# Optimization experiments

Measured on AMD Instinct MI355X. Metric: run time of the kernel, lower is better.

The kernel has to match this reference:

```python
import jax, jax.numpy as jnp
import numpy as np
from jax.scipy.special import logsumexp

NUM_CLASSES = 2
THRESHOLD = 0.35      # overlap_thresh
NEGPOS_RATIO = 7      # neg_pos
VAR0, VAR1 = 0.1, 0.2  # self.variance


def point_form(p):
    # (cx,cy,w,h) -> (x1,y1,x2,y2)
    return jnp.concatenate([p[:, :2] - p[:, 2:] / 2, p[:, :2] + p[:, 2:] / 2], axis=1)


def jaccard(a, b):
    # a: [T,4] xyxy, b: [P,4] xyxy -> IoU [T,P]
    lt = jnp.maximum(a[:, None, :2], b[None, :, :2])
    rb = jnp.minimum(a[:, None, 2:], b[None, :, 2:])
    wh = jnp.clip(rb - lt, 0.0)
    inter = wh[..., 0] * wh[..., 1]
    area_a = ((a[:, 2] - a[:, 0]) * (a[:, 3] - a[:, 1]))[:, None]
    area_b = ((b[:, 2] - b[:, 0]) * (b[:, 3] - b[:, 1]))[None, :]
    return inter / (area_a + area_b - inter)


def encode(matched, priors):
    # matched xyxy [P,4], priors cxcywh [P,4]
    g_cxcy = ((matched[:, :2] + matched[:, 2:]) / 2 - priors[:, :2]) / (VAR0 * priors[:, 2:])
    g_wh = jnp.log((matched[:, 2:] - matched[:, :2]) / priors[:, 2:]) / VAR1
    return jnp.concatenate([g_cxcy, g_wh], axis=1)


def encode_landm(matched, priors):
    m = matched.reshape(-1, 5, 2)  # [P,5,2]
    g = (m - priors[:, None, :2]) / (VAR0 * priors[:, None, 2:])
    return g.reshape(-1, 10)


def match_one(truths, labels, landms, priors):
    # truths [T,4] xyxy, labels [T], landms [T,10], priors [P,4] cxcywh
    overlaps = jaccard(truths, point_form(priors))  # [T,P]
    best_prior_overlap = overlaps.max(axis=1)       # [T]
    best_prior_idx = overlaps.argmax(axis=1)        # [T]
    valid_gt = best_prior_overlap >= 0.2            # hard-gt filter
    best_truth_overlap = overlaps.max(axis=0)       # [P]
    best_truth_idx = overlaps.argmax(axis=0)        # [P]
    # index_fill_(0, best_prior_idx[valid], 2): IoU <= 1 so scatter-max is exact
    best_truth_overlap = best_truth_overlap.at[best_prior_idx].max(
        jnp.where(valid_gt, 2.0, 0.0))
    best_truth_idx = best_truth_idx.at[best_prior_idx].set(jnp.arange(truths.shape[0]))
    matches = truths[best_truth_idx]                # [P,4]
    conf = jnp.where(best_truth_overlap < THRESHOLD, 0.0, labels[best_truth_idx])
    loc = encode(matches, priors)
    landm = encode_landm(landms[best_truth_idx], priors)
    any_valid = valid_gt.any()                      # early-return branch in torch match()
    loc = jnp.where(any_valid, loc, 0.0)
    conf = jnp.where(any_valid, conf, 0.0)
    landm = jnp.where(any_valid, landm, 0.0)
    return loc, conf.astype(jnp.int32), landm


def smooth_l1(x):
    ax = jnp.abs(x)
    return jnp.where(ax < 1.0, 0.5 * ax * ax, ax - 0.5)


def multibox_loss(loc_data, conf_data, landm_data, priors, targets):
    num_priors = priors.shape[0]
    # torch uses .data (detached) for matching/encoding targets
    truths = jax.lax.stop_gradient(targets[..., :4])
    landms_gt = jax.lax.stop_gradient(targets[..., 4:14])
    labels = jax.lax.stop_gradient(targets[..., 14])
    pri = jax.lax.stop_gradient(priors)
    loc_t, conf_t, landm_t = jax.vmap(match_one, in_axes=(0, 0, 0, None))(
        truths, labels, landms_gt, pri)  # [B,P,4], [B,P], [B,P,10]

    # landmark loss over conf_t > 0
    pos1 = conf_t > 0
    N1 = jnp.maximum(pos1.sum().astype(jnp.float32), 1.0)
    loss_landm = jnp.sum(smooth_l1(landm_data - landm_t) * pos1[..., None])

    # localization loss over conf_t != 0; conf_t[pos] = 1
    pos = conf_t != 0
    conf_t = jnp.where(pos, 1, conf_t)
    loss_l = jnp.sum(smooth_l1(loc_data - loc_t) * pos[..., None])

    # per-prior CE = logsumexp(logits) - logit[target]
    ce = logsumexp(conf_data, axis=-1) - jnp.take_along_axis(
        conf_data, conf_t[..., None], axis=-1)[..., 0]  # [B,P]
    # hard negative mining: zero positives, double-argsort rank trick
    rank_loss = jnp.where(pos, 0.0, ce)
    idx_rank = jnp.argsort(jnp.argsort(-rank_loss, axis=1), axis=1)
    num_pos = pos.sum(axis=1, keepdims=True)
    num_neg = jnp.minimum(NEGPOS_RATIO * num_pos, num_priors - 1)
    neg = idx_rank < num_neg
    loss_c = jnp.sum(jnp.where(pos | neg, ce, 0.0))

    N = jnp.maximum(num_pos.sum().astype(jnp.float32), 1.0)
    return loss_l / N, loss_c / N, loss_landm / N1


def setup_inputs() -> dict:
    key = jax.random.key(0)
    ks = jax.random.split(key, 8)
    B, P, T = 16, 32768, 64
    loc_data = jax.random.normal(ks[0], (B, P, 4), jnp.float32)
    conf_data = jax.random.normal(ks[1], (B, P, NUM_CLASSES), jnp.float32)
    landm_data = jax.random.normal(ks[2], (B, P, 10), jnp.float32)
    # priors: (cx,cy,w,h), all positive and in (0,1)
    cxcy = jax.random.uniform(ks[3], (P, 2), minval=0.05, maxval=0.95)
    wh = jax.random.uniform(ks[4], (P, 2), minval=0.02, maxval=0.3)
    priors = jnp.concatenate([cxcy, wh], axis=1)
    # targets: [x1,y1,x2,y2, 10 landmark coords, label]
    c = jax.random.uniform(ks[5], (B, T, 2), minval=0.15, maxval=0.85)
    s = jax.random.uniform(ks[6], (B, T, 2), minval=0.05, maxval=0.25)
    boxes = jnp.concatenate([c - s / 2, c + s / 2], axis=-1)
    lm = jax.random.uniform(ks[7], (B, T, 10))
    labels = jnp.ones((B, T, 1), jnp.float32)
    targets = jnp.concatenate([boxes, lm, labels], axis=-1)
    return {"loc_data": loc_data, "conf_data": conf_data,
            "landm_data": landm_data, "priors": priors, "targets": targets}


def reference(loc_data, conf_data, landm_data, priors, targets):
    return multibox_loss(loc_data, conf_data, landm_data, priors, targets)
```

## Files before the change

kernel.cpp:

```cpp
#include <hip/hip_runtime.h>
#include <math.h>

#define OVERLAP_THRESH 0.35f
#define VALID_THRESH   0.2f
#define NEGPOS         7
#define TMAX           64
#define NCHUNK         16
#define TPW            4
#define EPT            4
#define HB             2048
#define NC             4
#define NSCAN          32

__device__ __forceinline__ float sl1(float x) {
    float ax = fabsf(x);
    return ax < 1.0f ? 0.5f * ax * ax : ax - 0.5f;
}
__device__ __forceinline__ float frcp(float x) { return __builtin_amdgcn_rcpf(x); }

__device__ __forceinline__ void atomicMaxU8(unsigned char* addr, unsigned char val) {
    size_t a = (size_t)addr;
    unsigned* word = (unsigned*)(a & ~(size_t)3);
    int shift = (int)(a & 3) * 8;
    unsigned old = *word, assumed;
    do {
        unsigned cur = (old >> shift) & 0xFFu;
        if (cur >= val) break;
        assumed = old;
        unsigned nw = (old & ~(0xFFu << shift)) | ((unsigned)val << shift);
        old = atomicCAS(word, assumed, nw);
    } while (old != assumed);
}

__global__ void clear_ws_kernel(uint4* __restrict__ p, size_t n16) {
    size_t i = (size_t)blockIdx.x * blockDim.x + threadIdx.x;
    size_t stride = (size_t)gridDim.x * blockDim.x;
    uint4 z = make_uint4(0u, 0u, 0u, 0u);
    for (; i < n16; i += stride) p[i] = z;
}

__device__ __forceinline__ void select_coarse(const int* gh, int K, int lane, int add0,
                                              int* s_d1, int* s_r) {
    int base = lane * 32;
    int v[32]; int s = 0;
    #pragma unroll
    for (int j = 0; j < 32; j++) {
        int h = gh[base + j];
        if (base + j == 0) h += add0;
        v[j] = h; s += h;
    }
    int sfx = s;
    for (int off = 1; off < 64; off <<= 1) {
        int t = __shfl_down(sfx, off);
        if (lane + off < 64) sfx += t;
    }
    int ge = sfx;
    #pragma unroll
    for (int j = 0; j < 32; j++) {
        int gen = ge - v[j];
        if (ge >= K && gen < K) { *s_d1 = base + j; *s_r = K - gen; }
        ge = gen;
    }
}

__global__ void best_prior_partial_kernel(const float* __restrict__ priors,
                                          const float* __restrict__ targets,
                                          int P, int BT,
                                          unsigned long long* __restrict__ keys) {
    int wid  = blockIdx.x * (blockDim.x >> 6) + (threadIdx.x >> 6);
    int lane = threadIdx.x & 63;
    int ng    = (BT + TPW - 1) / TPW;
    int group = wid % ng;
    int chunk = wid / ng;
    int bt0   = group * TPW;

    float tx1[TPW], ty1[TPW], tx2[TPW], ty2[TPW], ta[TPW];
    #pragma unroll
    for (int j = 0; j < TPW; j++) {
        int bt = min(bt0 + j, BT - 1);
        const float* tg = targets + (size_t)bt * 15;
        tx1[j] = tg[0]; ty1[j] = tg[1]; tx2[j] = tg[2]; ty2[j] = tg[3];
        ta[j]  = (tx2[j] - tx1[j]) * (ty2[j] - ty1[j]);
    }

    int cs = (P + NCHUNK - 1) / NCHUNK;
    int p0 = chunk * cs;
    int pend = min(p0 + cs, P);
    float best[TPW]; int bestp[TPW];
    #pragma unroll
    for (int j = 0; j < TPW; j++) { best[j] = -1.0f; bestp[j] = p0; }

    for (int p = p0 + lane; p < pend; p += 64) {
        float4 pr = ((const float4*)priors)[p];
        float hw = pr.z * 0.5f, hh = pr.w * 0.5f;
        float px1 = pr.x - hw, py1 = pr.y - hh;
        float px2 = pr.x + hw, py2 = pr.y + hh;
        float pa = (px2 - px1) * (py2 - py1);
        #pragma unroll
        for (int j = 0; j < TPW; j++) {
            float iw = fmaxf(fminf(tx2[j], px2) - fmaxf(tx1[j], px1), 0.0f);
            float ih = fmaxf(fminf(ty2[j], py2) - fmaxf(ty1[j], py1), 0.0f);
            float inter = iw * ih;
            float iou = inter * frcp(ta[j] + pa - inter);
            if (iou > best[j]) { best[j] = iou; bestp[j] = p; }
        }
    }
    #pragma unroll
    for (int j = 0; j < TPW; j++) {
        unsigned long long key =
            ((unsigned long long)__float_as_uint(fmaxf(best[j], 0.0f)) << 32) |
            (unsigned long long)(0xFFFFFFFFu - (unsigned)bestp[j]);
        for (int off = 32; off; off >>= 1) {
            unsigned long long k2 = __shfl_down(key, off);
            if (k2 > key) key = k2;
        }
        if (lane == 0 && bt0 + j < BT) atomicMax(&keys[bt0 + j], key);
    }
}

__global__ void unpack_override_kernel(const unsigned long long* __restrict__ keys,
                                       int T, int BT, int P,
                                       unsigned char* __restrict__ ovr8,
                                       unsigned* __restrict__ vmask,
                                       int* __restrict__ av_arr) {
    int i = blockIdx.x * blockDim.x + threadIdx.x;
    if (i >= BT) return;
    unsigned long long k = keys[i];
    int bpi = (int)(0xFFFFFFFFu - (unsigned)(k & 0xFFFFFFFFull));
    float iou = __uint_as_float((unsigned)(k >> 32));
    int b = i / T, t = i % T;
    atomicMaxU8(&ovr8[(size_t)b * P + bpi], (unsigned char)(t + 1));
    if (iou >= VALID_THRESH) {
        atomicOr(&vmask[(size_t)b * (P >> 5) + (bpi >> 5)], 1u << (bpi & 31));
        atomicOr(&av_arr[b], 1);
    }
}

__global__ void match_loss_fused_kernel(const float* __restrict__ priors,
                                        const float* __restrict__ targets,
                                        const float* __restrict__ loc_data,
                                        const float* __restrict__ conf_data,
                                        const float* __restrict__ landm_data,
                                        const unsigned char* __restrict__ ovr8,
                                        const unsigned* __restrict__ vmask,
                                        const int* __restrict__ av_arr,
                                        int P, int T,
                                        float* __restrict__ rank_loss,
                                        int* __restrict__ ghist,
                                        int* __restrict__ num_pos,
                                        int* __restrict__ num_pos1,
                                        float* __restrict__ accb)
{
    int b   = blockIdx.y;
    int tid = threadIdx.x;
    int p0  = (blockIdx.x * blockDim.x + tid) * EPT;
    size_t base = (size_t)b * P + p0;

    __shared__ float4 s_box[TMAX];
    __shared__ float  s_ba[TMAX];
    __shared__ float  s_lab[TMAX];
    __shared__ int    s_hist[HB][NC];
    __shared__ float  s_ll, s_llm, s_cep;
    __shared__ int    s_np, s_np1;

    if (tid == 0) { s_ll = 0.f; s_llm = 0.f; s_cep = 0.f; s_np = 0; s_np1 = 0; }
    for (int i = tid; i < HB; i += blockDim.x)
        *(int4*)&s_hist[i][0] = make_int4(0, 0, 0, 0);
    if (tid < T) {
        const float* tg = targets + ((size_t)b * T + tid) * 15;
        float x1 = tg[0], y1 = tg[1], x2 = tg[2], y2 = tg[3];
        s_box[tid] = make_float4(x1, y1, x2, y2);
        s_ba[tid]  = (x2 - x1) * (y2 - y1);
        s_lab[tid] = tg[14];
    }
    __syncthreads();

    int hc = tid & (NC - 1);
    int av = av_arr[b];
    float ll_s = 0.f, cep_s = 0.f, llm_s = 0.f;
    int np_s = 0, np1_s = 0;

    if (p0 + EPT <= P) {
        float px1[EPT], py1[EPT], px2[EPT], py2[EPT], pa[EPT];
        float pcx[EPT], pcy[EPT], pw[EPT], ph[EPT];
        float best[EPT]; int btidx[EPT];
        #pragma unroll
        for (int j = 0; j < EPT; j++) {
            float4 pr = ((const float4*)priors)[p0 + j];
            float hw = pr.z * 0.5f, hh = pr.w * 0.5f;
            px1[j] = pr.x - hw; py1[j] = pr.y - hh;
            px2[j] = pr.x + hw; py2[j] = pr.y + hh;
            pa[j]  = (px2[j] - px1[j]) * (py2[j] - py1[j]);
            pcx[j] = pr.x; pcy[j] = pr.y; pw[j] = pr.z; ph[j] = pr.w;
            best[j] = -1.0f; btidx[j] = 0;
        }

        #pragma unroll 8
        for (int t = 0; t < TMAX; t++) {
            float4 box = s_box[t];
            float  ba  = s_ba[t];
            #pragma unroll
            for (int j = 0; j < EPT; j++) {
                float iw = fmaxf(fminf(box.z, px2[j]) - fmaxf(box.x, px1[j]), 0.0f);
                float ih = fmaxf(fminf(box.w, py2[j]) - fmaxf(box.y, py1[j]), 0.0f);
                float inter = iw * ih;
                float iou = inter * frcp(ba + pa[j] - inter);
                if (iou > best[j]) { best[j] = iou; btidx[j] = t; }
            }
        }

        unsigned ov4 = *(const unsigned*)&ovr8[base];
        unsigned vb  = vmask[(size_t)b * (P >> 5) + (p0 >> 5)] >> (p0 & 31);
        float cc[2 * EPT];
        *(float4*)&cc[0] = ((const float4*)(conf_data + base * 2))[0];
        *(float4*)&cc[4] = ((const float4*)(conf_data + base * 2))[1];

        float rl[EPT]; int btv[EPT]; float cev[EPT]; int posv[EPT];
        #pragma unroll
        for (int j = 0; j < EPT; j++) {
            int bt = btidx[j];
            int ov = (ov4 >> (8 * j)) & 0xFF;
            if (ov) bt = ov - 1;
            float bv = best[j];
            if ((vb >> j) & 1u) bv = 2.0f;
            btv[j] = bt;

            bool cond = (av && bv >= OVERLAP_THRESH);
            float lab = cond ? s_lab[bt] : 0.0f;
            int   ci  = (int)lab;
            bool  pos = cond && (ci != 0);
            posv[j] = pos;

            float c0 = cc[2 * j], c1 = cc[2 * j + 1];
            float mx = fmaxf(c0, c1);
            float lse = mx + __logf(1.0f + __expf(-fabsf(c0 - c1)));
            float ce  = lse - (pos ? c1 : c0);
            cev[j] = ce;
            rl[j] = pos ? 0.0f : fmaxf(ce, 0.0f);
            if (!pos) atomicAdd(&s_hist[__float_as_uint(rl[j]) >> 20][hc], 1);
        }
        *(float4*)&rank_loss[base] = *(float4*)rl;

        #pragma unroll
        for (int j = 0; j < EPT; j++) {
            if (!posv[j]) continue;
            int bt = btv[j];
            size_t idx = base + j;
            float4 mb = s_box[bt];
            bool pos1 = ((int)s_lab[bt] > 0);

            float rx = frcp(0.1f * pw[j]), ry = frcp(0.1f * ph[j]);
            float gx = ((mb.x + mb.z) * 0.5f - pcx[j]) * rx;
            float gy = ((mb.y + mb.w) * 0.5f - pcy[j]) * ry;
            float gw = __logf((mb.z - mb.x) * frcp(pw[j])) * 5.0f;
            float gh = __logf((mb.w - mb.y) * frcp(ph[j])) * 5.0f;
            const float* ld = loc_data + idx * 4;
            ll_s += sl1(ld[0] - gx) + sl1(ld[1] - gy) + sl1(ld[2] - gw) + sl1(ld[3] - gh);
            cep_s += cev[j];
            np_s++;

            if (pos1) {
                const float* lmd = landm_data + idx * 10;
                const float* lm  = targets + ((size_t)b * T + bt) * 15 + 4;
                float s = 0.0f;
                #pragma unroll
                for (int k = 0; k < 5; k++) {
                    float gxl = (lm[2 * k]     - pcx[j]) * rx;
                    float gyl = (lm[2 * k + 1] - pcy[j]) * ry;
                    s += sl1(lmd[2 * k] - gxl) + sl1(lmd[2 * k + 1] - gyl);
                }
                llm_s += s;
                np1_s++;
            }
        }
    }

    if (np_s)  { atomicAdd(&s_ll, ll_s); atomicAdd(&s_cep, cep_s); atomicAdd(&s_np, np_s); }
    if (np1_s) { atomicAdd(&s_llm, llm_s); atomicAdd(&s_np1, np1_s); }
    __syncthreads();
    if (tid == 0) {
        if (s_np)  { atomicAdd(&num_pos[b], s_np);
                     atomicAdd(&accb[b * 3 + 0], s_ll);
                     atomicAdd(&accb[b * 3 + 2], s_cep); }
        if (s_np1) { atomicAdd(&num_pos1[b], s_np1);
                     atomicAdd(&accb[b * 3 + 1], s_llm); }
    }
    for (int i = tid; i < HB; i += blockDim.x) {
        int4 v4 = *(int4*)&s_hist[i][0];
        int v = v4.x + v4.y + v4.z + v4.w;
        if (v) atomicAdd(&ghist[(size_t)b * HB + i], v);
    }
}

__device__ __forceinline__ void select_digit(const int* hist, int nb, int tid,
                                             int* s_dig, int* s_r) {
    if (tid < 64) {
        int lane = tid;
        int per  = (nb >= 64) ? (nb >> 6) : 1;
        int base = lane * per;
        int v[4]; int s = 0;
        #pragma unroll
        for (int j = 0; j < 4; j++) {
            int idx = base + j;
            int h = (j < per && idx < nb) ? hist[idx] : 0;
            v[j] = h; s += h;
        }
        int sfx = s;
        for (int off = 1; off < 64; off <<= 1) {
            int t = __shfl_down(sfx, off);
            if (lane + off < 64) sfx += t;
        }
        int r  = *s_r;
        int ge = sfx;
        #pragma unroll
        for (int j = 0; j < 4; j++) {
            int gen = ge - v[j];
            int d   = base + j;
            if (j < per && d < nb && ge >= r && gen < r) { *s_dig = d; *s_r = r - gen; }
            ge = gen;
        }
    }
}

__global__ void topk_scan_kernel(const float* __restrict__ rank_loss,
                                 const int* __restrict__ num_pos,
                                 const int* __restrict__ ghist,
                                 int P,
                                 float* __restrict__ glist,
                                 int* __restrict__ gcnt,
                                 float* __restrict__ accS,
                                 int* __restrict__ accC) {
    int b    = blockIdx.y;
    int tid  = threadIdx.x;
    int lane = tid & 63;
    int wv   = tid >> 6;
    int np   = num_pos[b];
    long long Kll = (long long)np * NEGPOS;
    int K = (Kll > P - 1) ? (P - 1) : (int)Kll;
    if (K <= 0) return;

    __shared__ int   s_d1, s_rdummy;
    __shared__ int   s_lcnt, s_base;
    __shared__ float s_stage[1024];
    __shared__ float s_S[4];
    __shared__ int   s_C[4];

    if (tid == 0) s_lcnt = 0;
    if (wv == 0) select_coarse(ghist + (size_t)b * HB, K, lane, np, &s_d1, &s_rdummy);
    __syncthreads();
    int d1 = s_d1;
    unsigned hi_lim = ((unsigned)(d1 + 1)) << 20;

    const float4* v4 = (const float4*)(rank_loss + (size_t)b * P);
    int n4  = P >> 2;
    int per = (n4 + NSCAN - 1) / NSCAN;
    int i0  = blockIdx.x * per;
    int i1  = min(i0 + per, n4);

    float S = 0.f; int C = 0;
    if (d1 == 0) {
        for (int i = i0 + tid; i < i1; i += blockDim.x) {
            float4 x = v4[i];
            float xs[4] = {x.x, x.y, x.z, x.w};
            #pragma unroll
            for (int k = 0; k < 4; k++) {
                unsigned u = __float_as_uint(xs[k]);
                if (u >= hi_lim) { S += xs[k]; C++; }
            }
        }
    } else {
        for (int i = i0 + tid; i < i1; i += blockDim.x) {
            float4 x = v4[i];
            float xs[4] = {x.x, x.y, x.z, x.w};
            #pragma unroll
            for (int k = 0; k < 4; k++) {
                unsigned u = __float_as_uint(xs[k]);
                if (u >= hi_lim) { S += xs[k]; C++; }
                bool m = ((u >> 20) == (unsigned)d1);
                unsigned long long mk = __ballot(m);
                if (m) {
                    int leader = __ffsll((long long)mk) - 1;
                    int base = 0;
                    if (lane == leader) base = atomicAdd(&s_lcnt, __popcll(mk));
                    base = __shfl(base, leader);
                    int ofs = __popcll(mk & (((unsigned long long)1 << lane) - 1ull));
                    s_stage[base + ofs] = xs[k];
                }
            }
        }
    }
    for (int off = 32; off; off >>= 1) {
        S += __shfl_down(S, off);
        C += __shfl_down(C, off);
    }
    if (lane == 0) { s_S[wv] = S; s_C[wv] = C; }
    __syncthreads();
    if (tid == 0) {
        float St = 0.f; int Ct = 0;
        for (int i = 0; i < 4; i++) { St += s_S[i]; Ct += s_C[i]; }
        if (Ct) { atomicAdd(&accS[b], St); atomicAdd(&accC[b], Ct); }
        s_base = s_lcnt ? atomicAdd(&gcnt[b], s_lcnt) : 0;
    }
    __syncthreads();
    int lc = s_lcnt, gbase = s_base;
    float* gl = glist + (size_t)b * P;
    for (int i = tid; i < lc; i += blockDim.x) gl[gbase + i] = s_stage[i];
}

__global__ void topk_refine_finalize_kernel(const int* __restrict__ num_pos,
                                            const int* __restrict__ num_pos1,
                                            const float* __restrict__ accb,
                                            const int* __restrict__ ghist,
                                            int P, int B,
                                            const float* __restrict__ glist,
                                            const int* __restrict__ gcnt,
                                            const float* __restrict__ accS,
                                            const int* __restrict__ accC,
                                            float* __restrict__ accn,
                                            int* __restrict__ done_ctr,
                                            float* __restrict__ out) {
    int b    = blockIdx.x;
    int tid  = threadIdx.x;
    int lane = tid & 63;
    int wv   = tid >> 6;
    int np   = num_pos[b];
    long long Kll = (long long)np * NEGPOS;
    int K = (Kll > P - 1) ? (P - 1) : (int)Kll;

    __shared__ int   hist[256];
    __shared__ int   s_d1, s_r, s_dig;
    __shared__ float s_S[16];
    __shared__ int   s_C[16];
    __shared__ float s_res;

    if (tid == 0) s_res = 0.0f;
    __syncthreads();

    if (K > 0) {
        if (wv == 0) select_coarse(ghist + (size_t)b * HB, K, lane, np, &s_d1, &s_r);
        __syncthreads();
        int d1 = s_d1;

        if (d1 == 0) {
            if (tid == 0) s_res = accS[b];
            __syncthreads();
        } else {
            int lc = gcnt[b];
            const float* gl = glist + (size_t)b * P;

            unsigned pmask = 0u, pval = 0u;
            const int shf[3] = {12, 4, 0};
            const int nbk[3] = {256, 256, 16};
            int trips = (lc + blockDim.x - 1) / blockDim.x;
            for (int ps = 0; ps < 3; ps++) {
                int sh = shf[ps]; unsigned wm = (unsigned)(nbk[ps] - 1);
                if (tid < 256) hist[tid] = 0;
                __syncthreads();
                for (int tc = 0; tc < trips; tc++) {
                    int i = tc * blockDim.x + tid;
                    bool ok = (i < lc);
                    unsigned u = ok ? __float_as_uint(gl[i]) : 0u;
                    ok = ok && ((u & pmask) == pval);
                    unsigned d = (u >> sh) & wm;
                    unsigned long long m = __ballot(ok);
                    #pragma unroll
                    for (int bit = 0; bit < 8; bit++) {
                        unsigned long long bb = __ballot((d >> bit) & 1u);
                        m &= ((d >> bit) & 1u) ? bb : ~bb;
                    }
                    if (ok && lane == (__ffsll((long long)m) - 1))
                        atomicAdd(&hist[d], __popcll(m));
                }
                __syncthreads();
                select_digit(hist, nbk[ps], tid, &s_dig, &s_r);
                __syncthreads();
                pval  |= ((unsigned)s_dig) << sh;
                pmask |= wm << sh;
            }
            float tau = __uint_as_float((((unsigned)d1) << 20) | pval);

            float S = 0.f; int C = 0;
            for (int i = tid; i < lc; i += blockDim.x) {
                float x = gl[i];
                if (x > tau) { S += x; C++; }
            }
            for (int off = 32; off; off >>= 1) {
                S += __shfl_down(S, off);
                C += __shfl_down(C, off);
            }
            if (lane == 0) { s_S[wv] = S; s_C[wv] = C; }
            __syncthreads();
            if (tid == 0) {
                float St = accS[b]; int Ct = accC[b];
                int nw = blockDim.x >> 6;
                for (int i = 0; i < nw; i++) { St += s_S[i]; Ct += s_C[i]; }
                s_res = St + (float)(K - Ct) * tau;
            }
            __syncthreads();
        }
    }

    if (tid == 0) {
        accn[b] = s_res;
        __threadfence();
        if (atomicAdd(done_ctr, 1) == B - 1) {
            float cen = 0.f;
            for (int j = 0; j < B; j++) cen += atomicAdd(&accn[j], 0.0f);
            int tp = 0, tp1 = 0;
            float ll = 0.f, llm = 0.f, cep = 0.f;
            for (int j = 0; j < B; j++) {
                tp  += num_pos[j];
                tp1 += num_pos1[j];
                ll  += accb[j * 3 + 0];
                llm += accb[j * 3 + 1];
                cep += accb[j * 3 + 2];
            }
            float N  = fmaxf((float)tp, 1.0f);
            float N1 = fmaxf((float)tp1, 1.0f);
            out[0] = ll / N;
            out[1] = (cep + cen) / N;
            out[2] = llm / N1;
        }
    }
}

extern "C" void kernel_launch(void* const* d_in, const int* in_sizes, int n_in,
                              void* d_out, int out_size, void* d_ws, size_t ws_size,
                              hipStream_t stream) {
    const float* loc_data   = (const float*)d_in[0];
    const float* conf_data  = (const float*)d_in[1];
    const float* landm_data = (const float*)d_in[2];
    const float* priors     = (const float*)d_in[3];
    const float* targets    = (const float*)d_in[4];
    float* out = (float*)d_out;

    int P  = in_sizes[3] / 4;
    int BP = in_sizes[0] / 4;
    int B  = BP / P;
    int T  = in_sizes[4] / (B * 15);
    int BT = B * T;

    char* ws = (char*)d_ws;
    float* rank_loss = (float*)ws;                    size_t off = (size_t)B * P * sizeof(float);
    float* glist     = (float*)(ws + off);            off += (size_t)B * P * sizeof(float);
    unsigned char* ovr8 = (unsigned char*)(ws + off); off += (size_t)B * P;
    unsigned* vmask = (unsigned*)(ws + off); off += (size_t)B * (P >> 5) * sizeof(unsigned);
    int* ghist      = (int*)(ws + off);      off += (size_t)B * HB * sizeof(int);
    unsigned long long* keys = (unsigned long long*)(ws + off); off += (size_t)BT * sizeof(unsigned long long);
    int* av_arr     = (int*)(ws + off);      off += (size_t)B * sizeof(int);
    int* num_pos    = (int*)(ws + off);      off += (size_t)B * sizeof(int);
    int* num_pos1   = (int*)(ws + off);      off += (size_t)B * sizeof(int);
    float* accb     = (float*)(ws + off);    off += (size_t)B * 3 * sizeof(float);
    float* accn     = (float*)(ws + off);    off += (size_t)B * sizeof(float);
    int* gcnt       = (int*)(ws + off);      off += (size_t)B * sizeof(int);
    float* accS     = (float*)(ws + off);    off += (size_t)B * sizeof(float);
    int* accC       = (int*)(ws + off);      off += (size_t)B * sizeof(int);
    int* done_ctr   = (int*)(ws + off);      off += sizeof(int);

    size_t zbytes = (size_t)((char*)(done_ctr + 1) - (char*)ovr8);
    size_t n16 = (zbytes + 15) / 16;
    clear_ws_kernel<<<256, 256, 0, stream>>>((uint4*)ovr8, n16);

    int waves   = NCHUNK * ((BT + TPW - 1) / TPW);
    int blocks2 = (waves + 3) / 4;
    best_prior_partial_kernel<<<blocks2, 256, 0, stream>>>(priors, targets, P, BT, keys);

    unpack_override_kernel<<<(BT + 255) / 256, 256, 0, stream>>>(keys, T, BT, P,
                                                                 ovr8, vmask, av_arr);

    dim3 gm((P + 256 * EPT - 1) / (256 * EPT), B);
    match_loss_fused_kernel<<<gm, 256, 0, stream>>>(priors, targets, loc_data, conf_data,
                                                    landm_data, ovr8, vmask, av_arr, P, T,
                                                    rank_loss, ghist, num_pos, num_pos1, accb);

    dim3 gs(NSCAN, B);
    topk_scan_kernel<<<gs, 256, 0, stream>>>(rank_loss, num_pos, ghist, P,
                                             glist, gcnt, accS, accC);

    topk_refine_finalize_kernel<<<B, 1024, 0, stream>>>(num_pos, num_pos1, accb, ghist,
                                                        P, B, glist, gcnt, accS, accC,
                                                        accn, done_ctr, out);
}
```

Measured before the change: 105.9 us.

## Compute IoU matrix once and share per-prior and per-target argmax results

Replaces the separate per-target best-prior kernel with a single IoU pass that produces both the per-prior best target (stored to workspace) and the per-target best prior via wave shuffles, ballot and shared-memory reduction followed by atomics. The loss kernel then loads the stored best IoU and target index instead of recomputing all IoUs. This removes one full evaluation of the T×P IoU matrix at the cost of extra global traffic for the intermediate arrays and per-target wave reductions.

```diff
diff --git a/kernel.cpp b/kernel.cpp
--- a/kernel.cpp
+++ b/kernel.cpp
@@ -5,8 +5,6 @@
 #define VALID_THRESH   0.2f
 #define NEGPOS         7
 #define TMAX           64
-#define NCHUNK         16
-#define TPW            4
 #define EPT            4
 #define HB             2048
 #define NC             4
@@ -63,58 +61,90 @@
     }
 }
 
-__global__ void best_prior_partial_kernel(const float* __restrict__ priors,
-                                          const float* __restrict__ targets,
-                                          int P, int BT,
-                                          unsigned long long* __restrict__ keys) {
-    int wid  = blockIdx.x * (blockDim.x >> 6) + (threadIdx.x >> 6);
-    int lane = threadIdx.x & 63;
-    int ng    = (BT + TPW - 1) / TPW;
-    int group = wid % ng;
-    int chunk = wid / ng;
-    int bt0   = group * TPW;
-
-    float tx1[TPW], ty1[TPW], tx2[TPW], ty2[TPW], ta[TPW];
+__global__ void iou_all_kernel(const float* __restrict__ priors,
+                               const float* __restrict__ targets,
+                               int P, int T,
+                               float* __restrict__ biou,
+                               unsigned char* __restrict__ bt8,
+                               unsigned long long* __restrict__ keys) {
+    int b    = blockIdx.y;
+    int tid  = threadIdx.x;
+    int lane = tid & 63;
+    int wv   = tid >> 6;
+    int p0   = (blockIdx.x * blockDim.x + tid) * EPT;
+
+    __shared__ float4 s_box[TMAX];
+    __shared__ float  s_ba[TMAX];
+    __shared__ unsigned long long s_tkey[TMAX][4];
+
+    for (int i = tid; i < TMAX * 4; i += blockDim.x)
+        s_tkey[i >> 2][i & 3] = 0ull;
+    if (tid < T) {
+        const float* tg = targets + ((size_t)b * T + tid) * 15;
+        float x1 = tg[0], y1 = tg[1], x2 = tg[2], y2 = tg[3];
+        s_box[tid] = make_float4(x1, y1, x2, y2);
+        s_ba[tid]  = (x2 - x1) * (y2 - y1);
+    }
+    __syncthreads();
+
+    float px1[EPT], py1[EPT], px2[EPT], py2[EPT], pa[EPT];
+    float best[EPT]; int btidx[EPT];
     #pragma unroll
-    for (int j = 0; j < TPW; j++) {
-        int bt = min(bt0 + j, BT - 1);
-        const float* tg = targets + (size_t)bt * 15;
-        tx1[j] = tg[0]; ty1[j] = tg[1]; tx2[j] = tg[2]; ty2[j] = tg[3];
-        ta[j]  = (tx2[j] - tx1[j]) * (ty2[j] - ty1[j]);
-    }
-
-    int cs = (P + NCHUNK - 1) / NCHUNK;
-    int p0 = chunk * cs;
-    int pend = min(p0 + cs, P);
-    float best[TPW]; int bestp[TPW];
-    #pragma unroll
-    for (int j = 0; j < TPW; j++) { best[j] = -1.0f; bestp[j] = p0; }
-
-    for (int p = p0 + lane; p < pend; p += 64) {
+    for (int j = 0; j < EPT; j++) {
+        int p = min(p0 + j, P - 1);
         float4 pr = ((const float4*)priors)[p];
         float hw = pr.z * 0.5f, hh = pr.w * 0.5f;
-        float px1 = pr.x - hw, py1 = pr.y - hh;
-        float px2 = pr.x + hw, py2 = pr.y + hh;
-        float pa = (px2 - px1) * (py2 - py1);
-        #pragma unroll
-        for (int j = 0; j < TPW; j++) {
-            float iw = fmaxf(fminf(tx2[j], px2) - fmaxf(tx1[j], px1), 0.0f);
-            float ih = fmaxf(fminf(ty2[j], py2) - fmaxf(ty1[j], py1), 0.0f);
+        px1[j] = pr.x - hw; py1[j] = pr.y - hh;
+        px2[j] = pr.x + hw; py2[j] = pr.y + hh;
+        pa[j]  = (px2[j] - px1[j]) * (py2[j] - py1[j]);
+        best[j] = -1.0f; btidx[j] = 0;
+    }
+
+    #pragma unroll 4
+    for (int t = 0; t < TMAX; t++) {
+        float4 box = s_box[t];
+        float  ba  = s_ba[t];
+        float liou = -1.0f; int lj = 0;
+        #pragma unroll
+        for (int j = 0; j < EPT; j++) {
+            float iw = fmaxf(fminf(box.z, px2[j]) - fmaxf(box.x, px1[j]), 0.0f);
+            float ih = fmaxf(fminf(box.w, py2[j]) - fmaxf(box.y, py1[j]), 0.0f);
             float inter = iw * ih;
-            float iou = inter * frcp(ta[j] + pa - inter);
-            if (iou > best[j]) { best[j] = iou; bestp[j] = p; }
-        }
-    }
-    #pragma unroll
-    for (int j = 0; j < TPW; j++) {
-        unsigned long long key =
-            ((unsigned long long)__float_as_uint(fmaxf(best[j], 0.0f)) << 32) |
-            (unsigned long long)(0xFFFFFFFFu - (unsigned)bestp[j]);
-        for (int off = 32; off; off >>= 1) {
-            unsigned long long k2 = __shfl_down(key, off);
-            if (k2 > key) key = k2;
-        }
-        if (lane == 0 && bt0 + j < BT) atomicMax(&keys[bt0 + j], key);
+            float iou = inter * frcp(ba + pa[j] - inter);
+            if (iou > best[j]) { best[j] = iou; btidx[j] = t; }
+            if (iou > liou)    { liou = iou; lj = j; }
+        }
+        float wm = liou;
+        #pragma unroll
+        for (int off = 32; off; off >>= 1)
+            wm = fmaxf(wm, __shfl_xor(wm, off));
+        unsigned long long mk = __ballot(liou == wm);
+        int leader = __ffsll((long long)mk) - 1;
+        if (lane == leader) {
+            int lp = min(p0 + lj, P - 1);
+            s_tkey[t][wv] = ((unsigned long long)__float_as_uint(fmaxf(wm, 0.0f)) << 32) |
+                            (unsigned long long)(0xFFFFFFFFu - (unsigned)lp);
+        }
+    }
+    __syncthreads();
+    if (tid < T) {
+        unsigned long long k = s_tkey[tid][0];
+        #pragma unroll
+        for (int w = 1; w < 4; w++) if (s_tkey[tid][w] > k) k = s_tkey[tid][w];
+        atomicMax(&keys[b * T + tid], k);
+    }
+
+    if (p0 + EPT <= P) {
+        *(float4*)&biou[(size_t)b * P + p0] = make_float4(best[0], best[1], best[2], best[3]);
+        *(uchar4*)&bt8[(size_t)b * P + p0] =
+            make_uchar4((unsigned char)btidx[0], (unsigned char)btidx[1],
+                        (unsigned char)btidx[2], (unsigned char)btidx[3]);
+    } else {
+        for (int j = 0; j < EPT; j++)
+            if (p0 + j < P) {
+                biou[(size_t)b * P + p0 + j] = best[j];
+                bt8[(size_t)b * P + p0 + j] = (unsigned char)btidx[j];
+            }
     }
 }
 
@@ -136,20 +166,22 @@
     }
 }
 
-__global__ void match_loss_fused_kernel(const float* __restrict__ priors,
-                                        const float* __restrict__ targets,
-                                        const float* __restrict__ loc_data,
-                                        const float* __restrict__ conf_data,
-                                        const float* __restrict__ landm_data,
-                                        const unsigned char* __restrict__ ovr8,
-                                        const unsigned* __restrict__ vmask,
-                                        const int* __restrict__ av_arr,
-                                        int P, int T,
-                                        float* __restrict__ rank_loss,
-                                        int* __restrict__ ghist,
-                                        int* __restrict__ num_pos,
-                                        int* __restrict__ num_pos1,
-                                        float* __restrict__ accb)
+__global__ void loss_eval_kernel(const float* __restrict__ priors,
+                                 const float* __restrict__ targets,
+                                 const float* __restrict__ loc_data,
+                                 const float* __restrict__ conf_data,
+                                 const float* __restrict__ landm_data,
+                                 const float* __restrict__ biou,
+                                 const unsigned char* __restrict__ bt8,
+                                 const unsigned char* __restrict__ ovr8,
+                                 const unsigned* __restrict__ vmask,
+                                 const int* __restrict__ av_arr,
+                                 int P, int T,
+                                 float* __restrict__ rank_loss,
+                                 int* __restrict__ ghist,
+                                 int* __restrict__ num_pos,
+                                 int* __restrict__ num_pos1,
+                                 float* __restrict__ accb)
 {
     int b   = blockIdx.y;
     int tid = threadIdx.x;
@@ -157,7 +189,6 @@
     size_t base = (size_t)b * P + p0;
 
     __shared__ float4 s_box[TMAX];
-    __shared__ float  s_ba[TMAX];
     __shared__ float  s_lab[TMAX];
     __shared__ int    s_hist[HB][NC];
     __shared__ float  s_ll, s_llm, s_cep;
@@ -168,9 +199,7 @@
         *(int4*)&s_hist[i][0] = make_int4(0, 0, 0, 0);
     if (tid < T) {
         const float* tg = targets + ((size_t)b * T + tid) * 15;
-        float x1 = tg[0], y1 = tg[1], x2 = tg[2], y2 = tg[3];
-        s_box[tid] = make_float4(x1, y1, x2, y2);
-        s_ba[tid]  = (x2 - x1) * (y2 - y1);
+        s_box[tid] = make_float4(tg[0], tg[1], tg[2], tg[3]);
         s_lab[tid] = tg[14];
     }
     __syncthreads();
@@ -181,34 +210,8 @@
     int np_s = 0, np1_s = 0;
 
     if (p0 + EPT <= P) {
-        float px1[EPT], py1[EPT], px2[EPT], py2[EPT], pa[EPT];
-        float pcx[EPT], pcy[EPT], pw[EPT], ph[EPT];
-        float best[EPT]; int btidx[EPT];
-        #pragma unroll
-        for (int j = 0; j < EPT; j++) {
-            float4 pr = ((const float4*)priors)[p0 + j];
-            float hw = pr.z * 0.5f, hh = pr.w * 0.5f;
-            px1[j] = pr.x - hw; py1[j] = pr.y - hh;
-            px2[j] = pr.x + hw; py2[j] = pr.y + hh;
-            pa[j]  = (px2[j] - px1[j]) * (py2[j] - py1[j]);
-            pcx[j] = pr.x; pcy[j] = pr.y; pw[j] = pr.z; ph[j] = pr.w;
-            best[j] = -1.0f; btidx[j] = 0;
-        }
-
-        #pragma unroll 8
-        for (int t = 0; t < TMAX; t++) {
-            float4 box = s_box[t];
-            float  ba  = s_ba[t];
-            #pragma unroll
-            for (int j = 0; j < EPT; j++) {
-                float iw = fmaxf(fminf(box.z, px2[j]) - fmaxf(box.x, px1[j]), 0.0f);
-                float ih = fmaxf(fminf(box.w, py2[j]) - fmaxf(box.y, py1[j]), 0.0f);
-                float inter = iw * ih;
-                float iou = inter * frcp(ba + pa[j] - inter);
-                if (iou > best[j]) { best[j] = iou; btidx[j] = t; }
-            }
-        }
-
+        float bi4[EPT];  *(float4*)bi4 = *(const float4*)&biou[base];
+        unsigned bt4 = *(const unsigned*)&bt8[base];
         unsigned ov4 = *(const unsigned*)&ovr8[base];
         unsigned vb  = vmask[(size_t)b * (P >> 5) + (p0 >> 5)] >> (p0 & 31);
         float cc[2 * EPT];
@@ -218,10 +221,10 @@
         float rl[EPT]; int btv[EPT]; float cev[EPT]; int posv[EPT];
         #pragma unroll
         for (int j = 0; j < EPT; j++) {
-            int bt = btidx[j];
+            int bt = (bt4 >> (8 * j)) & 0xFF;
             int ov = (ov4 >> (8 * j)) & 0xFF;
             if (ov) bt = ov - 1;
-            float bv = best[j];
+            float bv = bi4[j];
             if ((vb >> j) & 1u) bv = 2.0f;
             btv[j] = bt;
 
@@ -248,12 +251,13 @@
             size_t idx = base + j;
             float4 mb = s_box[bt];
             bool pos1 = ((int)s_lab[bt] > 0);
-
-            float rx = frcp(0.1f * pw[j]), ry = frcp(0.1f * ph[j]);
-            float gx = ((mb.x + mb.z) * 0.5f - pcx[j]) * rx;
-            float gy = ((mb.y + mb.w) * 0.5f - pcy[j]) * ry;
-            float gw = __logf((mb.z - mb.x) * frcp(pw[j])) * 5.0f;
-            float gh = __logf((mb.w - mb.y) * frcp(ph[j])) * 5.0f;
+            float4 pr = ((const float4*)priors)[p0 + j];
+
+            float rx = frcp(0.1f * pr.z), ry = frcp(0.1f * pr.w);
+            float gx = ((mb.x + mb.z) * 0.5f - pr.x) * rx;
+            float gy = ((mb.y + mb.w) * 0.5f - pr.y) * ry;
+            float gw = __logf((mb.z - mb.x) * frcp(pr.z)) * 5.0f;
+            float gh = __logf((mb.w - mb.y) * frcp(pr.w)) * 5.0f;
             const float* ld = loc_data + idx * 4;
             ll_s += sl1(ld[0] - gx) + sl1(ld[1] - gy) + sl1(ld[2] - gw) + sl1(ld[3] - gh);
             cep_s += cev[j];
@@ -265,8 +269,8 @@
                 float s = 0.0f;
                 #pragma unroll
                 for (int k = 0; k < 5; k++) {
-                    float gxl = (lm[2 * k]     - pcx[j]) * rx;
-                    float gyl = (lm[2 * k + 1] - pcy[j]) * ry;
+                    float gxl = (lm[2 * k]     - pr.x) * rx;
+                    float gyl = (lm[2 * k + 1] - pr.y) * ry;
                     s += sl1(lmd[2 * k] - gxl) + sl1(lmd[2 * k + 1] - gyl);
                 }
                 llm_s += s;
@@ -543,6 +547,8 @@
     char* ws = (char*)d_ws;
     float* rank_loss = (float*)ws;                    size_t off = (size_t)B * P * sizeof(float);
     float* glist     = (float*)(ws + off);            off += (size_t)B * P * sizeof(float);
+    float* biou      = (float*)(ws + off);            off += (size_t)B * P * sizeof(float);
+    unsigned char* bt8 = (unsigned char*)(ws + off);  off += (size_t)B * P;
     unsigned char* ovr8 = (unsigned char*)(ws + off); off += (size_t)B * P;
     unsigned* vmask = (unsigned*)(ws + off); off += (size_t)B * (P >> 5) * sizeof(unsigned);
     int* ghist      = (int*)(ws + off);      off += (size_t)B * HB * sizeof(int);
@@ -561,17 +567,15 @@
     size_t n16 = (zbytes + 15) / 16;
     clear_ws_kernel<<<256, 256, 0, stream>>>((uint4*)ovr8, n16);
 
-    int waves   = NCHUNK * ((BT + TPW - 1) / TPW);
-    int blocks2 = (waves + 3) / 4;
-    best_prior_partial_kernel<<<blocks2, 256, 0, stream>>>(priors, targets, P, BT, keys);
+    dim3 gm((P + 256 * EPT - 1) / (256 * EPT), B);
+    iou_all_kernel<<<gm, 256, 0, stream>>>(priors, targets, P, T, biou, bt8, keys);
 
     unpack_override_kernel<<<(BT + 255) / 256, 256, 0, stream>>>(keys, T, BT, P,
                                                                  ovr8, vmask, av_arr);
 
-    dim3 gm((P + 256 * EPT - 1) / (256 * EPT), B);
-    match_loss_fused_kernel<<<gm, 256, 0, stream>>>(priors, targets, loc_data, conf_data,
-                                                    landm_data, ovr8, vmask, av_arr, P, T,
-                                                    rank_loss, ghist, num_pos, num_pos1, accb);
+    loss_eval_kernel<<<gm, 256, 0, stream>>>(priors, targets, loc_data, conf_data,
+                                             landm_data, biou, bt8, ovr8, vmask, av_arr,
+                                             P, T, rank_loss, ghist, num_pos, num_pos1, accb);
 
     dim3 gs(NSCAN, B);
     topk_scan_kernel<<<gs, 256, 0, stream>>>(rank_loss, num_pos, ghist, P,
```

Result: no change. 105.0 us (-0.9%).
